# Optimization experiments

Measured on AMD Instinct MI355X. Metric: run time of the kernel, lower is better.

## Reference

```python
import jax, jax.numpy as jnp
import numpy as np

EPS = 1e-5          # module's self.eps
CLAMP = 1e-8        # numerical floor for norms
MAX_EUCLID = 32.0   # rescale_to_max_euclid cap (best-effort reconstruction)


def _linner(u, v):
    # Lorentz inner product <u,v>_L = -u0*v0 + <u_s,v_s>, keepdims on last axis
    uv = jnp.sum(u * v, axis=-1, keepdims=True)
    return uv - 2.0 * u[..., :1] * v[..., :1]


def _centroid(x):
    # Lorentzian (weighted) centroid: mean then renormalize onto hyperboloid (k=1)
    avg = jnp.mean(x, axis=-2)
    denom = jnp.sqrt(jnp.clip(-_linner(avg, avg), CLAMP, None))
    return avg / denom


def _logmap(x, y):
    # log_x(y) on Lorentz model, k=1
    alpha = jnp.clip(-_linner(x, y), 1.0 + 1e-7, None)
    u = y - alpha * x
    unorm = jnp.sqrt(jnp.clip(_linner(u, u), CLAMP, None))
    return jnp.arccosh(alpha) * u / unorm


def _plus_origin(y):
    # y + o where o = (1, 0, ..., 0)
    return jnp.concatenate([y[..., :1] + 1.0, y[..., 1:]], axis=-1)


def _transp0back(y, v):
    # parallel transport T_{y->o}(v): v + <o,v>_L/(1 - <y,o>_L) * (y + o); <o,v>_L = -v0
    coef = -v[..., :1] / (1.0 + y[..., :1])
    return v + coef * _plus_origin(y)


def _transp0(y, v):
    # parallel transport T_{o->y}(v): v + <y,v>_L/(1 + y0) * (o + y)
    coef = _linner(y, v) / (1.0 + y[..., :1])
    return v + coef * _plus_origin(y)


def _expmap(x, u):
    # exp_x(u) on Lorentz model, k=1
    nu = jnp.sqrt(jnp.clip(_linner(u, u), CLAMP, None))
    return jnp.cosh(nu) * x + jnp.sinh(nu) * u / nu


def _rescale_to_max_euclid(x):
    n = jnp.sqrt(jnp.sum(x * x, axis=-1, keepdims=True))
    return x * jnp.minimum(1.0, MAX_EUCLID / jnp.maximum(n, CLAMP))


def setup_inputs() -> dict:
    key = jax.random.key(0)
    B, S, D = 64, 4096, 128
    raw = 0.5 * jax.random.normal(key, (B, S, D - 1), dtype=jnp.float32)
    time = jnp.sqrt(1.0 + jnp.sum(raw * raw, axis=-1, keepdims=True))
    x = jnp.concatenate([time, raw], axis=-1)  # points on the hyperboloid
    gamma = jnp.ones((D,), dtype=jnp.float32)
    beta = jnp.zeros((D,), dtype=jnp.float32).at[0].set(1.0)  # manifold origin
    return {"x": x, "gamma": gamma, "beta": beta}


def reference(x, gamma, beta):
    # Training-mode Lorentz batchnorm (3D input path)
    mean = _centroid(x)       # (B, D)
    mean = _centroid(mean)    # (D,)
    x_T = _logmap(mean, x)            # tangent vectors at mean, (B, S, D)
    x_T = _transp0back(mean, x_T)     # transport to tangent space at origin
    var = jnp.sqrt(jnp.var(x_T, axis=(0, 1)) + EPS)   # Frechet per-feature std, (D,)
    x_T = x_T * (gamma / (var + EPS))
    x_T = _rescale_to_max_euclid(x_T)
    x_T = _transp0(beta, x_T)         # transport to tangent space at beta
    return _expmap(beta, x_T)
```

## Files before the change

kernel.cpp:

```cpp
#include <hip/hip_runtime.h>
#include <math.h>

#define NB 64
#define NS 4096
#define ND 128
#define NPTS (NB * NS)
#define PPB 256
#define NBLK (NPTS / PPB)
#define EPSV 1e-5f
#define CLAMPV 1e-8f
#define MAXEUC 32.0f

__device__ __forceinline__ float rcp_f(float x) { return __builtin_amdgcn_rcpf(x); }

#define DPP_ADD(v, ctrl)                                                            \
    v += __int_as_float(__builtin_amdgcn_update_dpp(0, __float_as_int(v), (ctrl),   \
                                                    0xF, 0xF, true))

__device__ __forceinline__ float row16_sum(float v) {
    DPP_ADD(v, 0x128);
    DPP_ADD(v, 0x124);
    DPP_ADD(v, 0x122);
    DPP_ADD(v, 0x121);
    return v;
}

__global__ __launch_bounds__(256) void k1(const float4* __restrict__ x4,
                                          float4* __restrict__ part1) {
    const int b = blockIdx.x >> 3;
    const int c = blockIdx.x & 7;
    const int d4 = threadIdx.x & 31;
    const int g  = threadIdx.x >> 5;
    const int srow = c * 512 + g;
    const float4* p = x4 + ((long long)b * NS + srow) * 32 + d4;
    float4 acc = make_float4(0.f, 0.f, 0.f, 0.f);
#pragma unroll 4
    for (int i = 0; i < 64; ++i) {
        float4 v = p[(long long)i * 8 * 32];
        acc.x += v.x; acc.y += v.y; acc.z += v.z; acc.w += v.w;
    }
    __shared__ float4 red[256];
    red[threadIdx.x] = acc;
    __syncthreads();
    if (threadIdx.x < 32) {
        float4 r = red[threadIdx.x];
#pragma unroll
        for (int gg = 1; gg < 8; ++gg) {
            float4 v = red[gg * 32 + threadIdx.x];
            r.x += v.x; r.y += v.y; r.z += v.z; r.w += v.w;
        }
        part1[(long long)blockIdx.x * 32 + threadIdx.x] = r;
    }
}

__global__ __launch_bounds__(1024) void k2(const float* __restrict__ part1,
                                           float* __restrict__ meanG) {
    __shared__ float avgL[NB * ND];
    __shared__ float avg2L[ND];
    __shared__ float denomS;
    const int t = threadIdx.x;
    for (int idx = t; idx < NB * ND; idx += 1024) {
        int b = idx >> 7, d = idx & 127;
        float s = 0.f;
#pragma unroll
        for (int c = 0; c < 8; ++c) s += part1[((b << 3) + c) * ND + d];
        avgL[idx] = s * (1.0f / (float)NS);
    }
    __syncthreads();
    const int w = t >> 6, l = t & 63;
    for (int b = w; b < NB; b += 16) {
        float a0 = avgL[b * ND + l];
        float a1 = avgL[b * ND + 64 + l];
        float a00 = avgL[b * ND];
        float s = a0 * a0 + a1 * a1;
#pragma unroll
        for (int o = 32; o > 0; o >>= 1) s += __shfl_xor(s, o, 64);
        float denom = sqrtf(fmaxf(2.f * a00 * a00 - s, CLAMPV));
        avgL[b * ND + l] = a0 / denom;
        avgL[b * ND + 64 + l] = a1 / denom;
    }
    __syncthreads();
    if (t < ND) {
        float s = 0.f;
        for (int b = 0; b < NB; ++b) s += avgL[b * ND + t];
        avg2L[t] = s * (1.0f / (float)NB);
    }
    __syncthreads();
    if (w == 0) {
        float a0 = avg2L[l], a1 = avg2L[l + 64];
        float s = a0 * a0 + a1 * a1;
#pragma unroll
        for (int o = 32; o > 0; o >>= 1) s += __shfl_xor(s, o, 64);
        float a00 = avg2L[0];
        float denom = sqrtf(fmaxf(2.f * a00 * a00 - s, CLAMPV));
        if (l == 0) denomS = denom;
    }
    __syncthreads();
    if (t < ND) meanG[t] = avg2L[t] / denomS;
}

__device__ __forceinline__ void point_scalars16(const float4& xa, const float4& xb,
                                                const float4& wa, const float4& wb,
                                                float m0, float inv1pm0, int fl,
                                                float& fac, float& hcoef) {
    float ad = wa.x * xa.x + wa.y * xa.y + wa.z * xa.z + wa.w * xa.w
             + wb.x * xb.x + wb.y * xb.y + wb.z * xb.z + wb.w * xb.w;
    float px = (fl == 0) ? xa.x : 0.f;
    ad = row16_sum(ad);
    px = row16_sum(px);
    float alpha = fmaxf(ad, 1.0f + 1e-7f);
    float am1 = alpha * alpha - 1.f;
    float sq = sqrtf(fmaxf(am1, CLAMPV));
    fac = __logf(alpha + sq) * rcp_f(sq);
    hcoef = -fac * (alpha + px) * inv1pm0;
}

__global__ __launch_bounds__(256) void k3(const float4* __restrict__ x4,
                                          const float* __restrict__ meanG,
                                          float* __restrict__ part3) {
    const int fl = threadIdx.x & 15;
    const int pg = threadIdx.x >> 4;
    const float4* m4 = (const float4*)meanG;
    const float4 ma = m4[fl], mb = m4[fl + 16];
    const float m0 = meanG[0];
    const float inv1pm0 = rcp_f(1.f + m0);
    float4 wa = make_float4(-ma.x, -ma.y, -ma.z, -ma.w);
    float4 wb = make_float4(-mb.x, -mb.y, -mb.z, -mb.w);
    if (fl == 0) wa.x = ma.x;
    float4 sa = make_float4(0.f, 0.f, 0.f, 0.f), sb = sa, qa = sa, qb = sa;
    const long long base = (long long)blockIdx.x * PPB;
#pragma unroll 4
    for (int i = 0; i < PPB / 16; ++i) {
        long long p = base + (long long)i * 16 + pg;
        float4 xa = x4[p * 32 + fl];
        float4 xb = x4[p * 32 + fl + 16];
        float fac, hc;
        point_scalars16(xa, xb, wa, wb, m0, inv1pm0, fl, fac, hc);
        float t0 = fac * xa.x + hc * ma.x;
        float t1 = fac * xa.y + hc * ma.y;
        float t2 = fac * xa.z + hc * ma.z;
        float t3 = fac * xa.w + hc * ma.w;
        float t4 = fac * xb.x + hc * mb.x;
        float t5 = fac * xb.y + hc * mb.y;
        float t6 = fac * xb.z + hc * mb.z;
        float t7 = fac * xb.w + hc * mb.w;
        if (fl == 0) t0 = 0.f;
        sa.x += t0; sa.y += t1; sa.z += t2; sa.w += t3;
        sb.x += t4; sb.y += t5; sb.z += t6; sb.w += t7;
        qa.x += t0 * t0; qa.y += t1 * t1; qa.z += t2 * t2; qa.w += t3 * t3;
        qb.x += t4 * t4; qb.y += t5 * t5; qb.z += t6 * t6; qb.w += t7 * t7;
    }
    __shared__ float ls[16][ND];
    __shared__ float lq[16][ND];
    float* ps = &ls[pg][fl * 8];
    float* pq = &lq[pg][fl * 8];
    ps[0] = sa.x; ps[1] = sa.y; ps[2] = sa.z; ps[3] = sa.w;
    ps[4] = sb.x; ps[5] = sb.y; ps[6] = sb.z; ps[7] = sb.w;
    pq[0] = qa.x; pq[1] = qa.y; pq[2] = qa.z; pq[3] = qa.w;
    pq[4] = qb.x; pq[5] = qb.y; pq[6] = qb.z; pq[7] = qb.w;
    __syncthreads();
    if (threadIdx.x < ND) {
        int d = threadIdx.x;
        int slot = ((d & 63) >> 2) * 8 + (d >> 6) * 4 + (d & 3);
        float S = 0.f, Q = 0.f;
#pragma unroll
        for (int cc = 0; cc < 16; ++cc) { S += ls[cc][slot]; Q += lq[cc][slot]; }
        part3[blockIdx.x * (2 * ND) + d] = S;
        part3[blockIdx.x * (2 * ND) + ND + d] = Q;
    }
}

__global__ __launch_bounds__(1024) void k4(const float* __restrict__ part3,
                                           const float* __restrict__ gamma,
                                           float* __restrict__ scaleG) {
    const int t = threadIdx.x;
    const int d = t & 127, g = t >> 7;
    double S = 0.0, Q = 0.0;
    for (int b = g; b < NBLK; b += 8) {
        S += (double)part3[b * (2 * ND) + d];
        Q += (double)part3[b * (2 * ND) + ND + d];
    }
    __shared__ double sS[8][ND];
    __shared__ double sQ[8][ND];
    sS[g][d] = S; sQ[g][d] = Q;
    __syncthreads();
    if (t < ND) {
        double St = 0.0, Qt = 0.0;
#pragma unroll
        for (int gg = 0; gg < 8; ++gg) { St += sS[gg][d]; Qt += sQ[gg][d]; }
        const double N = (double)NPTS;
        double mu = St / N;
        double var = Qt / N - mu * mu;
        if (var < 0.0) var = 0.0;
        float stdv = sqrtf((float)var + EPSV);
        scaleG[d] = gamma[d] / (stdv + EPSV);
    }
}

__global__ __launch_bounds__(256) void k5(const float4* __restrict__ x4,
                                          const float* __restrict__ meanG,
                                          const float* __restrict__ scaleG,
                                          const float* __restrict__ betaG,
                                          float4* __restrict__ out4) {
    const int fl = threadIdx.x & 15;
    const int pg = threadIdx.x >> 4;
    const float4* m4 = (const float4*)meanG;
    const float4* s4 = (const float4*)scaleG;
    const float4* b4 = (const float4*)betaG;
    const float4 ma = m4[fl], mb = m4[fl + 16];
    const float4 sca = s4[fl], scb = s4[fl + 16];
    const float4 bta = b4[fl], btb = b4[fl + 16];
    const float m0 = meanG[0];
    const float b0 = betaG[0];
    const float inv1pm0 = rcp_f(1.f + m0);
    const float inv1pb0 = rcp_f(1.f + b0);
    float4 wa = make_float4(-ma.x, -ma.y, -ma.z, -ma.w);
    float4 wb = make_float4(-mb.x, -mb.y, -mb.z, -mb.w);
    if (fl == 0) wa.x = ma.x;
    const long long base = (long long)blockIdx.x * PPB;
#pragma unroll 4
    for (int i = 0; i < PPB / 16; ++i) {
        long long p = base + (long long)i * 16 + pg;
        float4 xa = x4[p * 32 + fl];
        float4 xb = x4[p * 32 + fl + 16];
        float fac, hc;
        point_scalars16(xa, xb, wa, wb, m0, inv1pm0, fl, fac, hc);
        float ts0 = sca.x * (fac * xa.x + hc * ma.x);
        float ts1 = sca.y * (fac * xa.y + hc * ma.y);
        float ts2 = sca.z * (fac * xa.z + hc * ma.z);
        float ts3 = sca.w * (fac * xa.w + hc * ma.w);
        float ts4 = scb.x * (fac * xb.x + hc * mb.x);
        float ts5 = scb.y * (fac * xb.y + hc * mb.y);
        float ts6 = scb.z * (fac * xb.z + hc * mb.z);
        float ts7 = scb.w * (fac * xb.w + hc * mb.w);
        if (fl == 0) ts0 = 0.f;
        float nn = ts0 * ts0 + ts1 * ts1 + ts2 * ts2 + ts3 * ts3
                 + ts4 * ts4 + ts5 * ts5 + ts6 * ts6 + ts7 * ts7;
        float bd = bta.x * ts0 + bta.y * ts1 + bta.z * ts2 + bta.w * ts3
                 + btb.x * ts4 + btb.y * ts5 + btb.z * ts6 + btb.w * ts7;
        nn = row16_sum(nn);
        bd = row16_sum(bd);
        float n = sqrtf(nn);
        float r = fminf(1.f, MAXEUC * rcp_f(fmaxf(n, CLAMPV)));
        float coef2 = r * bd * inv1pb0;
        float nu = fmaxf(r * n, 1e-4f);
        float e = __expf(nu);
        float ei = rcp_f(e);
        float ch = 0.5f * (e + ei);
        float sf = (0.5f * (e - ei)) * rcp_f(nu);
        float A = ch + sf * coef2;
        float Bc = sf * r;
        float4 oa, ob;
        oa.x = Bc * ts0 + A * bta.x;
        oa.y = Bc * ts1 + A * bta.y;
        oa.z = Bc * ts2 + A * bta.z;
        oa.w = Bc * ts3 + A * bta.w;
        ob.x = Bc * ts4 + A * btb.x;
        ob.y = Bc * ts5 + A * btb.y;
        ob.z = Bc * ts6 + A * btb.z;
        ob.w = Bc * ts7 + A * btb.w;
        if (fl == 0) oa.x += sf * coef2;
        out4[p * 32 + fl] = oa;
        out4[p * 32 + fl + 16] = ob;
    }
}

extern "C" void kernel_launch(void* const* d_in, const int* in_sizes, int n_in,
                              void* d_out, int out_size, void* d_ws, size_t ws_size,
                              hipStream_t stream) {
    const float* x = (const float*)d_in[0];
    const float* gamma = (const float*)d_in[1];
    const float* beta = (const float*)d_in[2];
    float* out = (float*)d_out;
    float* ws = (float*)d_ws;

    float* part1  = ws;
    float* meanG  = ws + 65536;
    float* scaleG = ws + 65536 + 128;
    float* part3  = ws + 65536 + 256;

    k1<<<NB * 8, 256, 0, stream>>>((const float4*)x, (float4*)part1);
    k2<<<1, 1024, 0, stream>>>(part1, meanG);
    k3<<<NBLK, 256, 0, stream>>>((const float4*)x, meanG, part3);
    k4<<<1, 1024, 0, stream>>>(part3, gamma, scaleG);
    k5<<<NBLK, 256, 0, stream>>>((const float4*)x, meanG, scaleG, beta, (float4*)out);
}
```

Before: 320.0 us.

## Cache per-point log-map scalars, spread reductions across blocks, split centroid kernel

k3 now writes each point's logmap factor and transport coefficient to a workspace buffer, and k5 reads them back, so k5 no longer recomputes the dot product, log and DPP reductions. The first pass uses one block per 256 points with a coalesced layout. The single-block centroid kernel is split into a per-batch kernel and a tiny final kernel. The variance reduction now runs one block per feature over a transposed partial layout instead of a single 1024-thread block. This adds a 2 MB scalar buffer write and read plus one more launch, in exchange for less serial reduction work and less ALU work in k5.

Result: faster. 287.5 us (-10.2%).

```diff
diff --git a/kernel.cpp b/kernel.cpp
--- a/kernel.cpp
+++ b/kernel.cpp
@@ -25,83 +25,9 @@
     return v;
 }
 
-__global__ __launch_bounds__(256) void k1(const float4* __restrict__ x4,
-                                          float4* __restrict__ part1) {
-    const int b = blockIdx.x >> 3;
-    const int c = blockIdx.x & 7;
-    const int d4 = threadIdx.x & 31;
-    const int g  = threadIdx.x >> 5;
-    const int srow = c * 512 + g;
-    const float4* p = x4 + ((long long)b * NS + srow) * 32 + d4;
-    float4 acc = make_float4(0.f, 0.f, 0.f, 0.f);
-#pragma unroll 4
-    for (int i = 0; i < 64; ++i) {
-        float4 v = p[(long long)i * 8 * 32];
-        acc.x += v.x; acc.y += v.y; acc.z += v.z; acc.w += v.w;
-    }
-    __shared__ float4 red[256];
-    red[threadIdx.x] = acc;
-    __syncthreads();
-    if (threadIdx.x < 32) {
-        float4 r = red[threadIdx.x];
-#pragma unroll
-        for (int gg = 1; gg < 8; ++gg) {
-            float4 v = red[gg * 32 + threadIdx.x];
-            r.x += v.x; r.y += v.y; r.z += v.z; r.w += v.w;
-        }
-        part1[(long long)blockIdx.x * 32 + threadIdx.x] = r;
-    }
-}
-
-__global__ __launch_bounds__(1024) void k2(const float* __restrict__ part1,
-                                           float* __restrict__ meanG) {
-    __shared__ float avgL[NB * ND];
-    __shared__ float avg2L[ND];
-    __shared__ float denomS;
-    const int t = threadIdx.x;
-    for (int idx = t; idx < NB * ND; idx += 1024) {
-        int b = idx >> 7, d = idx & 127;
-        float s = 0.f;
-#pragma unroll
-        for (int c = 0; c < 8; ++c) s += part1[((b << 3) + c) * ND + d];
-        avgL[idx] = s * (1.0f / (float)NS);
-    }
-    __syncthreads();
-    const int w = t >> 6, l = t & 63;
-    for (int b = w; b < NB; b += 16) {
-        float a0 = avgL[b * ND + l];
-        float a1 = avgL[b * ND + 64 + l];
-        float a00 = avgL[b * ND];
-        float s = a0 * a0 + a1 * a1;
-#pragma unroll
-        for (int o = 32; o > 0; o >>= 1) s += __shfl_xor(s, o, 64);
-        float denom = sqrtf(fmaxf(2.f * a00 * a00 - s, CLAMPV));
-        avgL[b * ND + l] = a0 / denom;
-        avgL[b * ND + 64 + l] = a1 / denom;
-    }
-    __syncthreads();
-    if (t < ND) {
-        float s = 0.f;
-        for (int b = 0; b < NB; ++b) s += avgL[b * ND + t];
-        avg2L[t] = s * (1.0f / (float)NB);
-    }
-    __syncthreads();
-    if (w == 0) {
-        float a0 = avg2L[l], a1 = avg2L[l + 64];
-        float s = a0 * a0 + a1 * a1;
-#pragma unroll
-        for (int o = 32; o > 0; o >>= 1) s += __shfl_xor(s, o, 64);
-        float a00 = avg2L[0];
-        float denom = sqrtf(fmaxf(2.f * a00 * a00 - s, CLAMPV));
-        if (l == 0) denomS = denom;
-    }
-    __syncthreads();
-    if (t < ND) meanG[t] = avg2L[t] / denomS;
-}
-
 __device__ __forceinline__ void point_scalars16(const float4& xa, const float4& xb,
                                                 const float4& wa, const float4& wb,
-                                                float m0, float inv1pm0, int fl,
+                                                float inv1pm0, int fl,
                                                 float& fac, float& hcoef) {
     float ad = wa.x * xa.x + wa.y * xa.y + wa.z * xa.z + wa.w * xa.w
              + wb.x * xb.x + wb.y * xb.y + wb.z * xb.z + wb.w * xb.w;
@@ -115,9 +41,80 @@
     hcoef = -fac * (alpha + px) * inv1pm0;
 }
 
+__global__ __launch_bounds__(256) void k1(const float4* __restrict__ x4,
+                                          float* __restrict__ part1) {
+    const int fl = threadIdx.x & 15;
+    const int pg = threadIdx.x >> 4;
+    const long long base = (long long)blockIdx.x * PPB;
+    float4 sa = make_float4(0.f, 0.f, 0.f, 0.f), sb = sa;
+#pragma unroll 4
+    for (int i = 0; i < PPB / 16; ++i) {
+        long long p = base + i * 16 + pg;
+        float4 xa = x4[p * 32 + fl];
+        float4 xb = x4[p * 32 + fl + 16];
+        sa.x += xa.x; sa.y += xa.y; sa.z += xa.z; sa.w += xa.w;
+        sb.x += xb.x; sb.y += xb.y; sb.z += xb.z; sb.w += xb.w;
+    }
+    __shared__ float ls[16][ND];
+    float* ps = &ls[pg][fl * 8];
+    ps[0] = sa.x; ps[1] = sa.y; ps[2] = sa.z; ps[3] = sa.w;
+    ps[4] = sb.x; ps[5] = sb.y; ps[6] = sb.z; ps[7] = sb.w;
+    __syncthreads();
+    if (threadIdx.x < ND) {
+        int d = threadIdx.x;
+        int slot = ((d & 63) >> 2) * 8 + (d >> 6) * 4 + (d & 3);
+        float S = 0.f;
+#pragma unroll
+        for (int cc = 0; cc < 16; ++cc) S += ls[cc][slot];
+        part1[blockIdx.x * ND + d] = S;
+    }
+}
+
+__global__ __launch_bounds__(64) void k2a(const float* __restrict__ part1,
+                                          float* __restrict__ avg1) {
+    const int b = blockIdx.x;
+    const int t = threadIdx.x;
+    float a0 = 0.f, a1 = 0.f;
+#pragma unroll
+    for (int c = 0; c < 16; ++c) {
+        a0 += part1[(b * 16 + c) * ND + t];
+        a1 += part1[(b * 16 + c) * ND + 64 + t];
+    }
+    a0 *= (1.0f / (float)NS);
+    a1 *= (1.0f / (float)NS);
+    float s = a0 * a0 + a1 * a1;
+#pragma unroll
+    for (int o = 32; o > 0; o >>= 1) s += __shfl_xor(s, o, 64);
+    float a00 = __shfl(a0, 0, 64);
+    float denom = sqrtf(fmaxf(2.f * a00 * a00 - s, CLAMPV));
+    avg1[b * ND + t] = a0 / denom;
+    avg1[b * ND + 64 + t] = a1 / denom;
+}
+
+__global__ __launch_bounds__(64) void k2b(const float* __restrict__ avg1,
+                                          float* __restrict__ meanG) {
+    const int t = threadIdx.x;
+    float a0 = 0.f, a1 = 0.f;
+    for (int b = 0; b < NB; ++b) {
+        a0 += avg1[b * ND + t];
+        a1 += avg1[b * ND + 64 + t];
+    }
+    a0 *= (1.0f / (float)NB);
+    a1 *= (1.0f / (float)NB);
+    float s = a0 * a0 + a1 * a1;
+#pragma unroll
+    for (int o = 32; o > 0; o >>= 1) s += __shfl_xor(s, o, 64);
+    float a00 = __shfl(a0, 0, 64);
+    float denom = sqrtf(fmaxf(2.f * a00 * a00 - s, CLAMPV));
+    meanG[t] = a0 / denom;
+    meanG[64 + t] = a1 / denom;
+}
+
 __global__ __launch_bounds__(256) void k3(const float4* __restrict__ x4,
                                           const float* __restrict__ meanG,
-                                          float* __restrict__ part3) {
+                                          float* __restrict__ p3S,
+                                          float* __restrict__ p3Q,
+                                          float2* __restrict__ fchG) {
     const int fl = threadIdx.x & 15;
     const int pg = threadIdx.x >> 4;
     const float4* m4 = (const float4*)meanG;
@@ -131,11 +128,12 @@
     const long long base = (long long)blockIdx.x * PPB;
 #pragma unroll 4
     for (int i = 0; i < PPB / 16; ++i) {
-        long long p = base + (long long)i * 16 + pg;
+        long long p = base + i * 16 + pg;
         float4 xa = x4[p * 32 + fl];
         float4 xb = x4[p * 32 + fl + 16];
         float fac, hc;
-        point_scalars16(xa, xb, wa, wb, m0, inv1pm0, fl, fac, hc);
+        point_scalars16(xa, xb, wa, wb, inv1pm0, fl, fac, hc);
+        if (fl == 0) fchG[p] = make_float2(fac, hc);
         float t0 = fac * xa.x + hc * ma.x;
         float t1 = fac * xa.y + hc * ma.y;
         float t2 = fac * xa.z + hc * ma.z;
@@ -165,32 +163,34 @@
         float S = 0.f, Q = 0.f;
 #pragma unroll
         for (int cc = 0; cc < 16; ++cc) { S += ls[cc][slot]; Q += lq[cc][slot]; }
-        part3[blockIdx.x * (2 * ND) + d] = S;
-        part3[blockIdx.x * (2 * ND) + ND + d] = Q;
-    }
-}
-
-__global__ __launch_bounds__(1024) void k4(const float* __restrict__ part3,
-                                           const float* __restrict__ gamma,
-                                           float* __restrict__ scaleG) {
+        p3S[d * NBLK + blockIdx.x] = S;
+        p3Q[d * NBLK + blockIdx.x] = Q;
+    }
+}
+
+__global__ __launch_bounds__(256) void k4(const float* __restrict__ p3S,
+                                          const float* __restrict__ p3Q,
+                                          const float* __restrict__ gamma,
+                                          float* __restrict__ scaleG) {
+    const int d = blockIdx.x;
     const int t = threadIdx.x;
-    const int d = t & 127, g = t >> 7;
-    double S = 0.0, Q = 0.0;
-    for (int b = g; b < NBLK; b += 8) {
-        S += (double)part3[b * (2 * ND) + d];
-        Q += (double)part3[b * (2 * ND) + ND + d];
-    }
-    __shared__ double sS[8][ND];
-    __shared__ double sQ[8][ND];
-    sS[g][d] = S; sQ[g][d] = Q;
+    const float4* vS = (const float4*)(p3S + d * NBLK);
+    const float4* vQ = (const float4*)(p3Q + d * NBLK);
+    float4 a = vS[t];
+    float4 b = vQ[t];
+    __shared__ double dredS[256];
+    __shared__ double dredQ[256];
+    dredS[t] = (double)a.x + (double)a.y + (double)a.z + (double)a.w;
+    dredQ[t] = (double)b.x + (double)b.y + (double)b.z + (double)b.w;
     __syncthreads();
-    if (t < ND) {
-        double St = 0.0, Qt = 0.0;
-#pragma unroll
-        for (int gg = 0; gg < 8; ++gg) { St += sS[gg][d]; Qt += sQ[gg][d]; }
+    for (int o = 128; o > 0; o >>= 1) {
+        if (t < o) { dredS[t] += dredS[t + o]; dredQ[t] += dredQ[t + o]; }
+        __syncthreads();
+    }
+    if (t == 0) {
         const double N = (double)NPTS;
-        double mu = St / N;
-        double var = Qt / N - mu * mu;
+        double mu = dredS[0] / N;
+        double var = dredQ[0] / N - mu * mu;
         if (var < 0.0) var = 0.0;
         float stdv = sqrtf((float)var + EPSV);
         scaleG[d] = gamma[d] / (stdv + EPSV);
@@ -201,6 +201,7 @@
                                           const float* __restrict__ meanG,
                                           const float* __restrict__ scaleG,
                                           const float* __restrict__ betaG,
+                                          const float2* __restrict__ fchG,
                                           float4* __restrict__ out4) {
     const int fl = threadIdx.x & 15;
     const int pg = threadIdx.x >> 4;
@@ -210,21 +211,16 @@
     const float4 ma = m4[fl], mb = m4[fl + 16];
     const float4 sca = s4[fl], scb = s4[fl + 16];
     const float4 bta = b4[fl], btb = b4[fl + 16];
-    const float m0 = meanG[0];
     const float b0 = betaG[0];
-    const float inv1pm0 = rcp_f(1.f + m0);
     const float inv1pb0 = rcp_f(1.f + b0);
-    float4 wa = make_float4(-ma.x, -ma.y, -ma.z, -ma.w);
-    float4 wb = make_float4(-mb.x, -mb.y, -mb.z, -mb.w);
-    if (fl == 0) wa.x = ma.x;
     const long long base = (long long)blockIdx.x * PPB;
 #pragma unroll 4
     for (int i = 0; i < PPB / 16; ++i) {
-        long long p = base + (long long)i * 16 + pg;
+        long long p = base + i * 16 + pg;
         float4 xa = x4[p * 32 + fl];
         float4 xb = x4[p * 32 + fl + 16];
-        float fac, hc;
-        point_scalars16(xa, xb, wa, wb, m0, inv1pm0, fl, fac, hc);
+        float2 fh = fchG[p];
+        float fac = fh.x, hc = fh.y;
         float ts0 = sca.x * (fac * xa.x + hc * ma.x);
         float ts1 = sca.y * (fac * xa.y + hc * ma.y);
         float ts2 = sca.z * (fac * xa.z + hc * ma.z);
@@ -275,13 +271,18 @@
     float* ws = (float*)d_ws;
 
     float* part1  = ws;
-    float* meanG  = ws + 65536;
-    float* scaleG = ws + 65536 + 128;
-    float* part3  = ws + 65536 + 256;
-
-    k1<<<NB * 8, 256, 0, stream>>>((const float4*)x, (float4*)part1);
-    k2<<<1, 1024, 0, stream>>>(part1, meanG);
-    k3<<<NBLK, 256, 0, stream>>>((const float4*)x, meanG, part3);
-    k4<<<1, 1024, 0, stream>>>(part3, gamma, scaleG);
-    k5<<<NBLK, 256, 0, stream>>>((const float4*)x, meanG, scaleG, beta, (float4*)out);
-}
+    float* avg1   = part1 + NBLK * ND;
+    float* meanG  = avg1 + NB * ND;
+    float* scaleG = meanG + ND;
+    float* p3S    = scaleG + ND;
+    float* p3Q    = p3S + ND * NBLK;
+    float2* fchG  = (float2*)(p3Q + ND * NBLK);
+
+    k1 <<<NBLK, 256, 0, stream>>>((const float4*)x, part1);
+    k2a<<<NB, 64, 0, stream>>>(part1, avg1);
+    k2b<<<1, 64, 0, stream>>>(avg1, meanG);
+    k3 <<<NBLK, 256, 0, stream>>>((const float4*)x, meanG, p3S, p3Q, fchG);
+    k4 <<<ND, 256, 0, stream>>>(p3S, p3Q, gamma, scaleG);
+    k5 <<<NBLK, 256, 0, stream>>>((const float4*)x, meanG, scaleG, beta, fchG,
+                                  (float4*)out);
+}
```
